# Kernel tuning notes

Hardware: AMD Instinct MI355X
Metric: run time of the kernel (lower is better)

The kernel has to match this reference:

```python
import jax, jax.numpy as jnp
import numpy as np

B, S, D = 2048, 200, 128  # batch, history length, embedding dim
H = 64                    # attention_units[0]

def setup_inputs() -> dict:
    key = jax.random.key(0)
    k1, k2, k3, k4, k5 = jax.random.split(key, 5)
    return {
        "target_item": jax.random.normal(k1, (B, D), dtype=jnp.float32),
        "history_sequence": jax.random.normal(k2, (B, S, D), dtype=jnp.float32),
        "mask": jax.random.randint(k3, (B, S), 0, 2, dtype=jnp.int32),
        "W1": jax.random.normal(k4, (4 * D, H), dtype=jnp.float32) * (1.0 / np.sqrt(4 * D)),
        "b1": jnp.zeros((H,), dtype=jnp.float32),
        "W2": jax.random.normal(k5, (H, 1), dtype=jnp.float32) * (1.0 / np.sqrt(H)),
        "b2": jnp.zeros((1,), dtype=jnp.float32),
    }

def reference(target_item, history_sequence, mask, W1, b1, W2, b2):
    b, s, d = history_sequence.shape
    t = jnp.broadcast_to(target_item[:, None, :], (b, s, d))  # [B,S,D]
    # concat(target, history, diff, product) -> [B,S,4D]
    x = jnp.concatenate(
        [t, history_sequence, t - history_sequence, t * history_sequence], axis=-1)
    h = jax.nn.relu(x @ W1 + b1)          # [B,S,H]
    w = (h @ W2 + b2)[..., 0]             # [B,S]
    m = mask.astype(w.dtype)
    w = w * m                              # zero out padded positions (pre-softmax, as in source)
    w = w + (-1e9) * (1.0 - m)             # mask for softmax
    w = jax.nn.softmax(w, axis=-1)
    return jnp.einsum('bs,bsd->bd', w, history_sequence)  # [B,D]
```

## Files before the change

kernel.cpp:

```cpp
#include <hip/hip_runtime.h>
#include <hip/hip_bf16.h>

typedef __attribute__((ext_vector_type(8))) short bf16x8;
typedef __attribute__((ext_vector_type(4))) float f32x4;

#define B_ 2048
#define S_ 200
#define D_ 128
#define H_ 64
#define LOG2E 1.44269504f
#define TR 16
#define TB 8192

#define WS_AC 0u
#define WS_WB 32768u
#define WS_MT 65536u

static __device__ __forceinline__ short f2bf_hw(float f) {
    return (short)__builtin_bit_cast(unsigned short, __float2bfloat16(f));
}

static __device__ __forceinline__ void gload16(const void* g, void* l) {
    __builtin_amdgcn_global_load_lds(
        (const __attribute__((address_space(1))) unsigned int*)g,
        (__attribute__((address_space(3))) unsigned int*)l, 16, 0, 0);
}

__global__ __launch_bounds__(128)
void prep_fold(const float* __restrict__ W1, char* __restrict__ ws)
{
    const int n = blockIdx.x;
    const int k = threadIdx.x;
    float a = W1[k * H_ + n];
    float b = W1[(128 + k) * H_ + n];
    float c = W1[(256 + k) * H_ + n];
    float d = W1[(384 + k) * H_ + n];
    ((float*)(ws + WS_AC))[n * 128 + k] = a + c;
    char* img = ws + WS_WB;
    const int sw = (n & 7) << 4;
    const int kk = k >> 3, e2 = (k & 7) * 2;
    *(short*)(img + n * 512 + ((kk * 16) ^ sw) + e2)        = f2bf_hw(b - c);
    *(short*)(img + n * 512 + (((16 + kk) * 16) ^ sw) + e2) = f2bf_hw(d);
}

__global__ __launch_bounds__(256)
void prep_ta(const float* __restrict__ tgt, const float* __restrict__ b1,
             char* __restrict__ ws)
{
    __shared__ float tl[4][128];
    const int tid = threadIdx.x;
    const int b0 = blockIdx.x * 4;
    if (tid < 128) {
        int bb = tid >> 5, q = tid & 31;
        *(float4*)&tl[bb][q * 4] = ((const float4*)(tgt + (size_t)(b0 + bb) * D_))[q];
    }
    __syncthreads();
    const int n = tid & 63, bb = tid >> 6;
    const float* ac = (const float*)(ws + WS_AC) + n * 128;
    float s = 0.f;
    #pragma unroll 8
    for (int d = 0; d < 128; ++d) s = fmaf(tl[bb][d], ac[d], s);
    ((float*)(ws + WS_MT + (size_t)(b0 + bb) * 2048u + 512u))[n] = s + b1[n];
}

__global__ __launch_bounds__(256)
void mask_build(const int* __restrict__ mask, const float* __restrict__ tgt,
                char* __restrict__ ws)
{
    const int lane = threadIdx.x & 63;
    const int wv   = threadIdx.x >> 6;
    const int b    = blockIdx.x * 4 + wv;
    const int* mp  = mask + (size_t)b * S_;
    char* mt = ws + WS_MT + (size_t)b * 2048u;
    int* lst = (int*)(mt + 1024);
    int cnt = 0, last = 0;
    #pragma unroll
    for (int c = 0; c < 4; ++c) {
        int s = c * 64 + lane;
        int m = (s < S_) ? mp[s] : 0;
        unsigned long long bal = __ballot(m != 0);
        if (m) lst[cnt + __builtin_popcountll(bal & ((1ull << lane) - 1ull))] = s;
        if (bal) last = c * 64 + (63 - __builtin_clzll(bal));
        cnt += __builtin_popcountll(bal);
    }
    int uni = 0;
    if (cnt == 0) { uni = 1; cnt = S_; }
    for (int p = cnt + lane; p < 208; p += 64) lst[p] = uni ? (S_ - 1) : last;
    if (uni)
        for (int p = lane; p < S_; p += 64) lst[p] = p;
    if (lane == 0) *(int*)(mt + 768) = cnt | (uni << 16);
    if (lane < 32) ((float4*)mt)[lane] = ((const float4*)(tgt + (size_t)b * D_))[lane];
}

__global__ __launch_bounds__(256) __attribute__((amdgpu_waves_per_eu(1, 1)))
void din_fused(const float* __restrict__ hist, const float* __restrict__ W2,
               const char* __restrict__ ws, float* __restrict__ out)
{
    __shared__ __align__(16) char L[139264];
    const int tid  = threadIdx.x;
    const int lane = tid & 63;
    const int wv   = tid >> 6;
    const int b    = blockIdx.x * 4 + wv;
    const int lo   = lane & 15;
    const int hi   = lane >> 4;
    char* Lm = L + 32768 + wv * 26624;

    f32x4 w2v[4];
    #pragma unroll
    for (int ng = 0; ng < 4; ++ng) {
        f32x4 wl = *(const f32x4*)(W2 + ng * 16 + hi * 4);
        w2v[ng] = (f32x4){wl[0] * LOG2E, wl[1] * LOG2E, wl[2] * LOG2E, wl[3] * LOG2E};
    }

    {
        const char* wsrc = ws + WS_WB + wv * 8192 + (size_t)lane * 16u;
        #pragma unroll
        for (int i = 0; i < 8; ++i)
            gload16(wsrc + i * 1024, L + wv * 8192 + i * 1024);
        const char* msrc = ws + WS_MT + (size_t)b * 2048u + (size_t)lane * 16u;
        gload16(msrc,        Lm);
        gload16(msrc + 1024, Lm + 1024);
    }
    asm volatile("s_waitcnt vmcnt(0)" ::: "memory");
    __syncthreads();

    const int cw  = *(const int*)(Lm + 768);
    const int cnt = cw & 0xffff;
    const int uni = cw >> 16;
    const int nt  = (cnt + 15) >> 4;
    const int* ll = (const int*)(Lm + 1024);

    f32x4 tav[4];
    #pragma unroll
    for (int ng = 0; ng < 4; ++ng)
        tav[ng] = *(const f32x4*)(Lm + 512 + (ng * 16 + hi * 4) * 4);
    f32x4 tp0[4], tp1[4];
    #pragma unroll
    for (int ks = 0; ks < 4; ++ks) {
        tp0[ks] = *(const f32x4*)(Lm + ks * 128 + hi * 32);
        tp1[ks] = *(const f32x4*)(Lm + ks * 128 + hi * 32 + 16);
    }

    int abase[4], akoff[8];
    #pragma unroll
    for (int ng = 0; ng < 4; ++ng) abase[ng] = (ng * 16 + lo) * 512;
    #pragma unroll
    for (int ks = 0; ks < 8; ++ks) akoff[ks] = (ks * 64 + hi * 16) ^ ((lo & 7) << 4);
    bf16x8 bfH[4][4];
    #pragma unroll
    for (int ks = 0; ks < 4; ++ks)
        #pragma unroll
        for (int ng = 0; ng < 4; ++ng)
            bfH[ks][ng] = *(const bf16x8*)(L + abase[ng] + akoff[ks]);

    const int rb = (lo * 512 + hi * 32) ^ ((lo & 7) << 4);
    char* BB0 = Lm + 2048;
    char* BB1 = Lm + 2048 + TB;
    char* BB2 = Lm + 2048 + 2 * TB;

    const char* hb = (const char*)hist + (size_t)b * (S_ * D_ * 4);
    const int cp = (lane & 31) * 16;
    const int h5 = lane >> 5;
    auto stage = [&](int t, char* bufp) {
        #pragma unroll
        for (int i = 0; i < 8; ++i) {
            int r = 2 * i + h5;
            int rr = ll[t * 16 + r];
            gload16(hb + (size_t)rr * 512 + (cp ^ ((r & 7) << 4)), bufp + i * 1024);
        }
    };
    stage(0, BB0);
    stage(nt > 1 ? 1 : 0, BB1);
    stage(nt > 2 ? 2 : nt - 1, BB2);

    float o[4][8];
    #pragma unroll
    for (int ks = 0; ks < 4; ++ks)
        #pragma unroll
        for (int e = 0; e < 8; ++e) o[ks][e] = 0.f;
    float l = 0.f, mx = -1e30f;

    #pragma unroll 1
    for (int t = 0; t < nt; ++t) {
        char* buf = (t % 3 == 0) ? BB0 : (t % 3 == 1) ? BB1 : BB2;
        asm volatile("s_waitcnt vmcnt(16)" ::: "memory");
        __builtin_amdgcn_sched_barrier(0);
        f32x4 h0[4], h1[4];
        #pragma unroll
        for (int ks = 0; ks < 4; ++ks) {
            int o4 = rb + ks * 128;
            h0[ks] = *(const f32x4*)(buf + o4);
            h1[ks] = *(const f32x4*)(buf + (o4 ^ 16));
        }
        asm volatile("s_waitcnt lgkmcnt(0)" ::: "memory");
        __builtin_amdgcn_sched_barrier(0);
        if (t + 1 < nt) {
            int ts = t + 3; if (ts > nt - 1) ts = nt - 1;
            stage(ts, buf);
        }
        f32x4 acc[4];
        #pragma unroll
        for (int ng = 0; ng < 4; ++ng) acc[ng] = (f32x4){0.f, 0.f, 0.f, 0.f};
        #pragma unroll
        for (int ks = 0; ks < 4; ++ks) {
            bf16x8 bh, bt;
            #pragma unroll
            for (int e = 0; e < 4; ++e) {
                bh[e]     = f2bf_hw(h0[ks][e]);
                bh[e + 4] = f2bf_hw(h1[ks][e]);
                bt[e]     = f2bf_hw(tp0[ks][e] * h0[ks][e]);
                bt[e + 4] = f2bf_hw(tp1[ks][e] * h1[ks][e]);
            }
            #pragma unroll
            for (int ng = 0; ng < 4; ++ng)
                acc[ng] = __builtin_amdgcn_mfma_f32_16x16x32_bf16(bfH[ks][ng], bh, acc[ng], 0, 0, 0);
            #pragma unroll
            for (int ng = 0; ng < 4; ++ng) {
                bf16x8 afd = *(const bf16x8*)(L + abase[ng] + akoff[ks + 4]);
                acc[ng] = __builtin_amdgcn_mfma_f32_16x16x32_bf16(afd, bt, acc[ng], 0, 0, 0);
            }
        }
        float s0 = 0.f, s1 = 0.f, s2 = 0.f, s3 = 0.f;
        #pragma unroll
        for (int e = 0; e < 4; ++e) {
            s0 = fmaf(fmaxf(acc[0][e] + tav[0][e], 0.f), w2v[0][e], s0);
            s1 = fmaf(fmaxf(acc[1][e] + tav[1][e], 0.f), w2v[1][e], s1);
            s2 = fmaf(fmaxf(acc[2][e] + tav[2][e], 0.f), w2v[2][e], s2);
            s3 = fmaf(fmaxf(acc[3][e] + tav[3][e], 0.f), w2v[3][e], s3);
        }
        float sum = (s0 + s1) + (s2 + s3);
        sum += __shfl_xor(sum, 16);
        sum += __shfl_xor(sum, 32);
        const bool valid = (t * 16 + lo) < cnt;
        float lg = uni ? (valid ? 0.f : -1e30f) : (valid ? sum : -1e30f);
        float tm = lg;
        tm = fmaxf(tm, __shfl_xor(tm, 1));
        tm = fmaxf(tm, __shfl_xor(tm, 2));
        tm = fmaxf(tm, __shfl_xor(tm, 4));
        tm = fmaxf(tm, __shfl_xor(tm, 8));
        if (tm > mx + 11.5f) {
            float rsc = exp2f(mx - tm);
            #pragma unroll
            for (int ks = 0; ks < 4; ++ks)
                #pragma unroll
                for (int e = 0; e < 8; ++e) o[ks][e] *= rsc;
            l *= rsc;
            mx = tm;
        }
        float p = valid ? exp2f(lg - mx) : 0.f;
        l += p;
        #pragma unroll
        for (int ks = 0; ks < 4; ++ks) {
            o[ks][0] = fmaf(p, h0[ks][0], o[ks][0]);
            o[ks][1] = fmaf(p, h0[ks][1], o[ks][1]);
            o[ks][2] = fmaf(p, h0[ks][2], o[ks][2]);
            o[ks][3] = fmaf(p, h0[ks][3], o[ks][3]);
            o[ks][4] = fmaf(p, h1[ks][0], o[ks][4]);
            o[ks][5] = fmaf(p, h1[ks][1], o[ks][5]);
            o[ks][6] = fmaf(p, h1[ks][2], o[ks][6]);
            o[ks][7] = fmaf(p, h1[ks][3], o[ks][7]);
        }
    }

    #pragma unroll
    for (int ks = 0; ks < 4; ++ks)
        #pragma unroll
        for (int e = 0; e < 8; ++e) {
            float v = o[ks][e];
            v += __shfl_xor(v, 1);
            v += __shfl_xor(v, 2);
            v += __shfl_xor(v, 4);
            v += __shfl_xor(v, 8);
            o[ks][e] = v;
        }
    l += __shfl_xor(l, 1);
    l += __shfl_xor(l, 2);
    l += __shfl_xor(l, 4);
    l += __shfl_xor(l, 8);

    const float inv = 1.0f / l;
    if (lo == 0) {
        float* op = out + (size_t)b * D_ + hi * 8;
        #pragma unroll
        for (int ks = 0; ks < 4; ++ks) {
            *(f32x4*)(op + ks * 32)     = (f32x4){o[ks][0] * inv, o[ks][1] * inv,
                                                  o[ks][2] * inv, o[ks][3] * inv};
            *(f32x4*)(op + ks * 32 + 4) = (f32x4){o[ks][4] * inv, o[ks][5] * inv,
                                                  o[ks][6] * inv, o[ks][7] * inv};
        }
    }
}

extern "C" void kernel_launch(void* const* d_in, const int* in_sizes, int n_in,
                              void* d_out, int out_size, void* d_ws, size_t ws_size,
                              hipStream_t stream) {
    const float* tgt  = (const float*)d_in[0];
    const float* hist = (const float*)d_in[1];
    const int*   mask = (const int*)d_in[2];
    const float* W1   = (const float*)d_in[3];
    const float* b1   = (const float*)d_in[4];
    const float* W2   = (const float*)d_in[5];
    const float* b2   = (const float*)d_in[6];
    (void)b2;
    float* out = (float*)d_out;
    char* ws = (char*)d_ws;

    prep_fold<<<64, 128, 0, stream>>>(W1, ws);
    prep_ta<<<B_ / 4, 256, 0, stream>>>(tgt, b1, ws);
    mask_build<<<B_ / 4, 256, 0, stream>>>(mask, tgt, ws);
    din_fused<<<B_ / 4, 256, 0, stream>>>(hist, W2, ws, out);
}
```

Baseline: 56.39 us.

## Fuse target projection and mask compaction into main attention kernel

```diff
diff --git a/kernel.cpp b/kernel.cpp
--- a/kernel.cpp
+++ b/kernel.cpp
@@ -14,7 +14,6 @@
 
 #define WS_AC 0u
 #define WS_WB 32768u
-#define WS_MT 65536u
 
 static __device__ __forceinline__ short f2bf_hw(float f) {
     return (short)__builtin_bit_cast(unsigned short, __float2bfloat16(f));
@@ -35,7 +34,7 @@
     float b = W1[(128 + k) * H_ + n];
     float c = W1[(256 + k) * H_ + n];
     float d = W1[(384 + k) * H_ + n];
-    ((float*)(ws + WS_AC))[n * 128 + k] = a + c;
+    ((float*)(ws + WS_AC))[k * 64 + n] = a + c;
     char* img = ws + WS_WB;
     const int sw = (n & 7) << 4;
     const int kk = k >> 3, e2 = (k & 7) * 2;
@@ -43,58 +42,11 @@
     *(short*)(img + n * 512 + (((16 + kk) * 16) ^ sw) + e2) = f2bf_hw(d);
 }
 
-__global__ __launch_bounds__(256)
-void prep_ta(const float* __restrict__ tgt, const float* __restrict__ b1,
-             char* __restrict__ ws)
-{
-    __shared__ float tl[4][128];
-    const int tid = threadIdx.x;
-    const int b0 = blockIdx.x * 4;
-    if (tid < 128) {
-        int bb = tid >> 5, q = tid & 31;
-        *(float4*)&tl[bb][q * 4] = ((const float4*)(tgt + (size_t)(b0 + bb) * D_))[q];
-    }
-    __syncthreads();
-    const int n = tid & 63, bb = tid >> 6;
-    const float* ac = (const float*)(ws + WS_AC) + n * 128;
-    float s = 0.f;
-    #pragma unroll 8
-    for (int d = 0; d < 128; ++d) s = fmaf(tl[bb][d], ac[d], s);
-    ((float*)(ws + WS_MT + (size_t)(b0 + bb) * 2048u + 512u))[n] = s + b1[n];
-}
-
-__global__ __launch_bounds__(256)
-void mask_build(const int* __restrict__ mask, const float* __restrict__ tgt,
-                char* __restrict__ ws)
-{
-    const int lane = threadIdx.x & 63;
-    const int wv   = threadIdx.x >> 6;
-    const int b    = blockIdx.x * 4 + wv;
-    const int* mp  = mask + (size_t)b * S_;
-    char* mt = ws + WS_MT + (size_t)b * 2048u;
-    int* lst = (int*)(mt + 1024);
-    int cnt = 0, last = 0;
-    #pragma unroll
-    for (int c = 0; c < 4; ++c) {
-        int s = c * 64 + lane;
-        int m = (s < S_) ? mp[s] : 0;
-        unsigned long long bal = __ballot(m != 0);
-        if (m) lst[cnt + __builtin_popcountll(bal & ((1ull << lane) - 1ull))] = s;
-        if (bal) last = c * 64 + (63 - __builtin_clzll(bal));
-        cnt += __builtin_popcountll(bal);
-    }
-    int uni = 0;
-    if (cnt == 0) { uni = 1; cnt = S_; }
-    for (int p = cnt + lane; p < 208; p += 64) lst[p] = uni ? (S_ - 1) : last;
-    if (uni)
-        for (int p = lane; p < S_; p += 64) lst[p] = p;
-    if (lane == 0) *(int*)(mt + 768) = cnt | (uni << 16);
-    if (lane < 32) ((float4*)mt)[lane] = ((const float4*)(tgt + (size_t)b * D_))[lane];
-}
-
 __global__ __launch_bounds__(256) __attribute__((amdgpu_waves_per_eu(1, 1)))
-void din_fused(const float* __restrict__ hist, const float* __restrict__ W2,
-               const char* __restrict__ ws, float* __restrict__ out)
+void din_fused(const float* __restrict__ tgt, const float* __restrict__ hist,
+               const int* __restrict__ mask, const float* __restrict__ W2,
+               const float* __restrict__ b1, const char* __restrict__ ws,
+               float* __restrict__ out)
 {
     __shared__ __align__(16) char L[139264];
     const int tid  = threadIdx.x;
@@ -105,41 +57,66 @@
     const int hi   = lane >> 4;
     char* Lm = L + 32768 + wv * 26624;
 
+    {
+        const char* wsrc = ws + WS_WB + wv * 8192 + (size_t)lane * 16u;
+        #pragma unroll
+        for (int i = 0; i < 8; ++i)
+            gload16(wsrc + i * 1024, L + wv * 8192 + i * 1024);
+    }
+
     f32x4 w2v[4];
     #pragma unroll
     for (int ng = 0; ng < 4; ++ng) {
         f32x4 wl = *(const f32x4*)(W2 + ng * 16 + hi * 4);
         w2v[ng] = (f32x4){wl[0] * LOG2E, wl[1] * LOG2E, wl[2] * LOG2E, wl[3] * LOG2E};
     }
-
+    f32x4 tp0[4], tp1[4];
+    #pragma unroll
+    for (int ks = 0; ks < 4; ++ks) {
+        tp0[ks] = *(const f32x4*)(tgt + (size_t)b * D_ + ks * 32 + hi * 8);
+        tp1[ks] = *(const f32x4*)(tgt + (size_t)b * D_ + ks * 32 + hi * 8 + 4);
+    }
+
+    int* lst = (int*)(Lm + 1024);
+    int cnt = 0, uni = 0;
     {
-        const char* wsrc = ws + WS_WB + wv * 8192 + (size_t)lane * 16u;
-        #pragma unroll
-        for (int i = 0; i < 8; ++i)
-            gload16(wsrc + i * 1024, L + wv * 8192 + i * 1024);
-        const char* msrc = ws + WS_MT + (size_t)b * 2048u + (size_t)lane * 16u;
-        gload16(msrc,        Lm);
-        gload16(msrc + 1024, Lm + 1024);
-    }
+        const int* mp = mask + (size_t)b * S_;
+        int last = 0;
+        #pragma unroll
+        for (int c = 0; c < 4; ++c) {
+            int s = c * 64 + lane;
+            int m = (s < S_) ? mp[s] : 0;
+            unsigned long long bal = __ballot(m != 0);
+            if (m) lst[cnt + __builtin_popcountll(bal & ((1ull << lane) - 1ull))] = s;
+            if (bal) last = c * 64 + (63 - __builtin_clzll(bal));
+            cnt += __builtin_popcountll(bal);
+        }
+        if (cnt == 0) { uni = 1; cnt = S_; }
+        for (int p = cnt + lane; p < 208; p += 64) lst[p] = uni ? (S_ - 1) : last;
+        if (uni)
+            for (int p = lane; p < S_; p += 64) lst[p] = p;
+    }
+
+    {
+        const float* ak = (const float*)(ws + WS_AC) + lane;
+        const float* tb = tgt + (size_t)b * D_;
+        float ta = 0.f;
+        #pragma unroll 16
+        for (int d = 0; d < 128; ++d)
+            ta = fmaf(tb[d], ak[d * 64], ta);
+        ta += b1[lane];
+        *(float*)(Lm + 512 + lane * 4) = ta;
+    }
+    f32x4 tav[4];
+    #pragma unroll
+    for (int ng = 0; ng < 4; ++ng)
+        tav[ng] = *(const f32x4*)(Lm + 512 + (ng * 16 + hi * 4) * 4);
+
     asm volatile("s_waitcnt vmcnt(0)" ::: "memory");
     __syncthreads();
 
-    const int cw  = *(const int*)(Lm + 768);
-    const int cnt = cw & 0xffff;
-    const int uni = cw >> 16;
-    const int nt  = (cnt + 15) >> 4;
+    const int nt = (cnt + 15) >> 4;
     const int* ll = (const int*)(Lm + 1024);
-
-    f32x4 tav[4];
-    #pragma unroll
-    for (int ng = 0; ng < 4; ++ng)
-        tav[ng] = *(const f32x4*)(Lm + 512 + (ng * 16 + hi * 4) * 4);
-    f32x4 tp0[4], tp1[4];
-    #pragma unroll
-    for (int ks = 0; ks < 4; ++ks) {
-        tp0[ks] = *(const f32x4*)(Lm + ks * 128 + hi * 32);
-        tp1[ks] = *(const f32x4*)(Lm + ks * 128 + hi * 32 + 16);
-    }
 
     int abase[4], akoff[8];
     #pragma unroll
@@ -306,7 +283,5 @@
     char* ws = (char*)d_ws;
 
     prep_fold<<<64, 128, 0, stream>>>(W1, ws);
-    prep_ta<<<B_ / 4, 256, 0, stream>>>(tgt, b1, ws);
-    mask_build<<<B_ / 4, 256, 0, stream>>>(mask, tgt, ws);
-    din_fused<<<B_ / 4, 256, 0, stream>>>(hist, W2, ws, out);
-}
+    din_fused<<<B_ / 4, 256, 0, stream>>>(tgt, hist, mask, W2, b1, ws, out);
+}
```

New measurement: 51.34 us. 9.0% less time.
